# Performance work log

Hardware: AMD Instinct MI355X
Metric: run time of the kernel (lower is better)

Reference implementation:

```python
import jax, jax.numpy as jnp
import numpy as np

NEURON_CDECAY = 0.5
NEURON_VDECAY = 0.75
NEURON_VTH = 0.5

B, D_IN, T = 4096, 1024, 16
H1, H2, D_OUT = 1024, 1024, 512


def setup_inputs() -> dict:
    key = jax.random.key(0)
    ks = jax.random.split(key, 7)
    def lin(k, fan_in, shape):
        bound = 1.0 / np.sqrt(fan_in)
        return jax.random.uniform(k, shape, jnp.float32, -bound, bound)
    # input spikes: binary-ish spike trains in [0,1)
    in_pop_spikes = (jax.random.uniform(ks[0], (B, D_IN, T)) < 0.3).astype(jnp.float32)
    return {
        "in_pop_spikes": in_pop_spikes,
        "W1": lin(ks[1], D_IN, (H1, D_IN)), "b1": lin(ks[2], D_IN, (H1,)),
        "W2": lin(ks[3], H1, (H2, H1)), "b2": lin(ks[4], H1, (H2,)),
        "Wo": lin(ks[5], H2, (D_OUT, H2)), "bo": lin(ks[6], H2, (D_OUT,)),
        "batch_size": B,
    }


def pseudo_spike(volt):
    return (volt > NEURON_VTH).astype(volt.dtype)


def clif_step(x, W, b, cur, volt, spk):
    cur = cur * NEURON_CDECAY + x @ W.T + b
    volt = volt * NEURON_VDECAY * (1.0 - spk) + cur
    spk = pseudo_spike(volt)
    return cur, volt, spk


def reference(in_pop_spikes, W1, b1, W2, b2, Wo, bo, batch_size):
    bsz = batch_size
    xs = jnp.transpose(in_pop_spikes, (2, 0, 1))  # [T, B, D_in]
    z = lambda d: jnp.zeros((bsz, d), jnp.float32)
    init = (z(H1), z(H1), z(H1), z(H2), z(H2), z(H2), z(D_OUT), z(D_OUT), z(D_OUT))

    def step(state, x):
        c1, v1, s1, c2, v2, s2, co, vo, so = state
        c1, v1, s1 = clif_step(x, W1, b1, c1, v1, s1)
        c2, v2, s2 = clif_step(s1, W2, b2, c2, v2, s2)
        co, vo, so = clif_step(s2, Wo, bo, co, vo, so)
        return (c1, v1, s1, c2, v2, s2, co, vo, so), so

    _, spikes = jax.lax.scan(step, init, xs)  # spikes: [T, B, D_out]
    return jnp.sum(spikes, axis=0) / T
```

## Files before the change

### kernel.cpp

```cpp
#include <hip/hip_runtime.h>


typedef float floatx4 __attribute__((ext_vector_type(4)));

static constexpr int BSZ   = 4096;
static constexpr int D_IN  = 1024;
static constexpr int H1    = 1024;
static constexpr int D_OUT = 512;
static constexpr int M_ROWS = BSZ * 16;

__global__ void pack_x(const float* __restrict__ X, float* __restrict__ A) {
    const int P = blockIdx.x * 256 + threadIdx.x;
    const int b = P >> 10, d = P & 1023;
    const float4* xp = (const float4*)(X + (size_t)P * 16);
    float4 x0 = xp[0], x1 = xp[1], x2 = xp[2], x3 = xp[3];
    const float v[16] = {x0.x, x0.y, x0.z, x0.w, x1.x, x1.y, x1.z, x1.w,
                         x2.x, x2.y, x2.z, x2.w, x3.x, x3.y, x3.z, x3.w};
#pragma unroll
    for (int t = 0; t < 16; ++t)
        A[((size_t)(b * 16 + t)) * 1024 + d] = v[t];
}

__global__ __launch_bounds__(256, 2) void gemm_np(
    const float* __restrict__ A,
    const float* __restrict__ W,
    float* __restrict__ C,
    int N) {
#pragma clang fp contract(off)
    __shared__ float As[256 * 33];
    __shared__ float Ws[128 * 32];

    const int tid = threadIdx.x;
    const int tx = tid & 15;
    const int ty = tid >> 4;
    const int m0 = blockIdx.x * 256, n0 = blockIdx.y * 128;

    const float* Ag = A + (size_t)(m0 + tid) * 1024;
    const int wn = tid & 127, wq0 = (tid >> 7) * 4;
    const float* Wg = W + (size_t)(n0 + wn) * 1024 + wq0 * 4;
    const int wswz = (wn >> 3) & 7;

    float acc[16][8] = {};

    for (int kt = 0; kt < 32; ++kt) {
        const int k0 = kt * 32;
        floatx4 av[8], wv[4];
#pragma unroll
        for (int c = 0; c < 8; ++c)
            av[c] = *(const floatx4*)(Ag + k0 + c * 4);
#pragma unroll
        for (int q = 0; q < 4; ++q)
            wv[q] = *(const floatx4*)(Wg + k0 + q * 4);
        __syncthreads();
#pragma unroll
        for (int c = 0; c < 8; ++c)
            *(floatx4*)&As[tid * 33 + c * 4] = av[c];
#pragma unroll
        for (int q = 0; q < 4; ++q)
            *(floatx4*)&Ws[wn * 32 + (((wq0 + q) ^ wswz) * 4)] = wv[q];
        __syncthreads();

#pragma unroll
        for (int kq = 0; kq < 8; ++kq) {
            const int wch = (kq ^ (tx & 7)) * 4;
            const int ach = kq * 4;
            floatx4 w4[8], a4[8];
#pragma unroll
            for (int j = 0; j < 8; ++j)
                w4[j] = *(const floatx4*)&Ws[(tx * 8 + j) * 32 + wch];
#pragma unroll
            for (int i = 0; i < 8; ++i)
                a4[i] = *(const floatx4*)&As[(ty * 16 + i) * 33 + ach];
#pragma unroll
            for (int kk = 0; kk < 4; ++kk)
#pragma unroll
                for (int i = 0; i < 8; ++i)
#pragma unroll
                    for (int j = 0; j < 8; ++j)
                        acc[i][j] = __builtin_fmaf(a4[i][kk], w4[j][kk], acc[i][j]);
#pragma unroll
            for (int i = 0; i < 8; ++i)
                a4[i] = *(const floatx4*)&As[(ty * 16 + 8 + i) * 33 + ach];
#pragma unroll
            for (int kk = 0; kk < 4; ++kk)
#pragma unroll
                for (int i = 0; i < 8; ++i)
#pragma unroll
                    for (int j = 0; j < 8; ++j)
                        acc[8 + i][j] = __builtin_fmaf(a4[i][kk], w4[j][kk], acc[8 + i][j]);
        }
    }

#pragma unroll
    for (int i = 0; i < 16; ++i) {
        floatx4 s0 = {acc[i][0], acc[i][1], acc[i][2], acc[i][3]};
        floatx4 s1 = {acc[i][4], acc[i][5], acc[i][6], acc[i][7]};
        float* cp = C + (size_t)(m0 + ty * 16 + i) * N + n0 + tx * 8;
        *(floatx4*)cp       = s0;
        *(floatx4*)(cp + 4) = s1;
    }
}

__global__ void recur_hidden(float* __restrict__ Z, const float* __restrict__ bias) {
#pragma clang fp contract(off)
    const int idx = blockIdx.x * 256 + threadIdx.x;
    const int n = idx & 1023, b = idx >> 10;
    const float bb = bias[n];
    float c = 0.f, v = 0.f, s = 0.f;
#pragma unroll
    for (int t = 0; t < 16; ++t) {
        const size_t p = (size_t)(b * 16 + t) * 1024 + n;
        const float z = Z[p];
        const float t1 = c * 0.5f;
        const float t2 = t1 + z;
        c = t2 + bb;
        const float u1 = v * 0.75f;
        const float u2 = u1 * (1.0f - s);
        v = u2 + c;
        s = (v > 0.5f) ? 1.0f : 0.0f;
        Z[p] = s;
    }
}

__global__ void recur_out(const float* __restrict__ Z, const float* __restrict__ bias,
                          float* __restrict__ Out) {
#pragma clang fp contract(off)
    const int idx = blockIdx.x * 256 + threadIdx.x;
    const int n = idx & 511, b = idx >> 9;
    const float bb = bias[n];
    float c = 0.f, v = 0.f, s = 0.f, acm = 0.f;
#pragma unroll
    for (int t = 0; t < 16; ++t) {
        const float z = Z[(size_t)(b * 16 + t) * 512 + n];
        const float t1 = c * 0.5f;
        const float t2 = t1 + z;
        c = t2 + bb;
        const float u1 = v * 0.75f;
        const float u2 = u1 * (1.0f - s);
        v = u2 + c;
        s = (v > 0.5f) ? 1.0f : 0.0f;
        acm += s;
    }
    Out[(size_t)b * 512 + n] = acm * 0.0625f;
}

extern "C" void kernel_launch(void* const* d_in, const int* in_sizes, int n_in,
                              void* d_out, int out_size, void* d_ws, size_t ws_size,
                              hipStream_t stream) {
    const float* X  = (const float*)d_in[0];
    const float* W1 = (const float*)d_in[1];
    const float* b1 = (const float*)d_in[2];
    const float* W2 = (const float*)d_in[3];
    const float* b2 = (const float*)d_in[4];
    const float* Wo = (const float*)d_in[5];
    const float* bo = (const float*)d_in[6];

    char* ws = (char*)d_ws;
    float* buf0 = (float*)ws;
    float* buf1 = (float*)(ws + (256ull << 20));

    pack_x<<<(BSZ * D_IN) / 256, 256, 0, stream>>>(X, buf0);

    gemm_np<<<dim3(M_ROWS / 256, H1 / 128), 256, 0, stream>>>(buf0, W1, buf1, H1);
    recur_hidden<<<(BSZ * H1) / 256, 256, 0, stream>>>(buf1, b1);
    gemm_np<<<dim3(M_ROWS / 256, H1 / 128), 256, 0, stream>>>(buf1, W2, buf0, H1);
    recur_hidden<<<(BSZ * H1) / 256, 256, 0, stream>>>(buf0, b2);
    gemm_np<<<dim3(M_ROWS / 256, D_OUT / 128), 256, 0, stream>>>(buf0, Wo, buf1, D_OUT);
    recur_out<<<(BSZ * D_OUT) / 256, 256, 0, stream>>>(buf1, bo, (float*)d_out);
}
```

Measured before the change: 4.382 ms.

## Transpose GEMM shared-memory tiles to k-major layout with interleaved W columns

The A and W tiles in LDS are stored k-major (As[k][m], Ws[k][n]) instead of row-major with padding and XOR swizzling. W columns are permuted so each thread reads two aligned float4 vectors per k step. The inner loop now walks k one element at a time with aligned 128-bit LDS reads, replacing the misaligned 33-stride A reads. In exchange, global-to-LDS stores become scalar transposing writes, and the occupancy hint moves to waves_per_eu.

```diff
diff --git a/kernel.cpp b/kernel.cpp
--- a/kernel.cpp
+++ b/kernel.cpp
@@ -21,14 +21,21 @@
         A[((size_t)(b * 16 + t)) * 1024 + d] = v[t];
 }
 
-__global__ __launch_bounds__(256, 2) void gemm_np(
+__device__ __forceinline__ int wcol(int n) {
+    const int c = n >> 2, l = n & 3;
+    return ((c & 1) << 6) | ((c >> 1) << 2) | l;
+}
+
+__global__ __launch_bounds__(256)
+__attribute__((amdgpu_waves_per_eu(2, 2)))
+void gemm_np(
     const float* __restrict__ A,
     const float* __restrict__ W,
     float* __restrict__ C,
     int N) {
 #pragma clang fp contract(off)
-    __shared__ float As[256 * 33];
-    __shared__ float Ws[128 * 32];
+    __shared__ float As[32][256];
+    __shared__ float Ws[32][128];
 
     const int tid = threadIdx.x;
     const int tx = tid & 15;
@@ -36,9 +43,9 @@
     const int m0 = blockIdx.x * 256, n0 = blockIdx.y * 128;
 
     const float* Ag = A + (size_t)(m0 + tid) * 1024;
-    const int wn = tid & 127, wq0 = (tid >> 7) * 4;
-    const float* Wg = W + (size_t)(n0 + wn) * 1024 + wq0 * 4;
-    const int wswz = (wn >> 3) & 7;
+    const int wn = tid & 127, wkh = (tid >> 7) * 16;
+    const float* Wg = W + (size_t)(n0 + wn) * 1024 + wkh;
+    const int wc = wcol(wn);
 
     float acc[16][8] = {};
 
@@ -54,40 +61,37 @@
         __syncthreads();
 #pragma unroll
         for (int c = 0; c < 8; ++c)
-            *(floatx4*)&As[tid * 33 + c * 4] = av[c];
+#pragma unroll
+            for (int e = 0; e < 4; ++e)
+                As[c * 4 + e][tid] = av[c][e];
 #pragma unroll
         for (int q = 0; q < 4; ++q)
-            *(floatx4*)&Ws[wn * 32 + (((wq0 + q) ^ wswz) * 4)] = wv[q];
+#pragma unroll
+            for (int e = 0; e < 4; ++e)
+                Ws[wkh + q * 4 + e][wc] = wv[q][e];
         __syncthreads();
 
 #pragma unroll
-        for (int kq = 0; kq < 8; ++kq) {
-            const int wch = (kq ^ (tx & 7)) * 4;
-            const int ach = kq * 4;
-            floatx4 w4[8], a4[8];
+        for (int kk = 0; kk < 32; ++kk) {
+            floatx4 w0 = *(const floatx4*)&Ws[kk][tx * 4];
+            floatx4 w1 = *(const floatx4*)&Ws[kk][64 + tx * 4];
 #pragma unroll
-            for (int j = 0; j < 8; ++j)
-                w4[j] = *(const floatx4*)&Ws[(tx * 8 + j) * 32 + wch];
+            for (int c = 0; c < 4; ++c) {
+                floatx4 a4 = *(const floatx4*)&As[kk][ty * 16 + c * 4];
 #pragma unroll
-            for (int i = 0; i < 8; ++i)
-                a4[i] = *(const floatx4*)&As[(ty * 16 + i) * 33 + ach];
-#pragma unroll
-            for (int kk = 0; kk < 4; ++kk)
-#pragma unroll
-                for (int i = 0; i < 8; ++i)
-#pragma unroll
-                    for (int j = 0; j < 8; ++j)
-                        acc[i][j] = __builtin_fmaf(a4[i][kk], w4[j][kk], acc[i][j]);
-#pragma unroll
-            for (int i = 0; i < 8; ++i)
-                a4[i] = *(const floatx4*)&As[(ty * 16 + 8 + i) * 33 + ach];
-#pragma unroll
-            for (int kk = 0; kk < 4; ++kk)
-#pragma unroll
-                for (int i = 0; i < 8; ++i)
-#pragma unroll
-                    for (int j = 0; j < 8; ++j)
-                        acc[8 + i][j] = __builtin_fmaf(a4[i][kk], w4[j][kk], acc[8 + i][j]);
+                for (int e = 0; e < 4; ++e) {
+                    const float ai = a4[e];
+                    const int i = c * 4 + e;
+                    acc[i][0] = __builtin_fmaf(ai, w0[0], acc[i][0]);
+                    acc[i][1] = __builtin_fmaf(ai, w0[1], acc[i][1]);
+                    acc[i][2] = __builtin_fmaf(ai, w0[2], acc[i][2]);
+                    acc[i][3] = __builtin_fmaf(ai, w0[3], acc[i][3]);
+                    acc[i][4] = __builtin_fmaf(ai, w1[0], acc[i][4]);
+                    acc[i][5] = __builtin_fmaf(ai, w1[1], acc[i][5]);
+                    acc[i][6] = __builtin_fmaf(ai, w1[2], acc[i][6]);
+                    acc[i][7] = __builtin_fmaf(ai, w1[3], acc[i][7]);
+                }
+            }
         }
     }
 
```

Result: slower. 6.666 ms (+52.1%).
